# Performance work log

Measured on AMD Instinct MI355X. Metric: run time of the kernel, lower is better.

## Reference

```python
import jax, jax.numpy as jnp
import numpy as np

FEATURE_DIM = 256
NUM_STEPS = 3
NUM_GRAPHS = 2048
ATOMS_PER_GRAPH = 64
TOTAL_ATOMS = NUM_GRAPHS * ATOMS_PER_GRAPH


def setup_inputs() -> dict:
    key = jax.random.key(0)
    k_x, k1, k2, k3, k4 = jax.random.split(key, 5)
    H = FEATURE_DIM
    s = 1.0 / np.sqrt(H)
    x = jax.random.normal(k_x, (TOTAL_ATOMS, H), dtype=jnp.float32)
    batch = jnp.repeat(jnp.arange(NUM_GRAPHS, dtype=jnp.int64), ATOMS_PER_GRAPH)
    sizes = jnp.full((NUM_GRAPHS,), ATOMS_PER_GRAPH, dtype=jnp.int64)
    # LSTM params (PyTorch layout: gates ordered i, f, g, o)
    W_ih = jax.random.uniform(k1, (4 * H, H), jnp.float32, -s, s)
    W_hh = jax.random.uniform(k2, (4 * H, H), jnp.float32, -s, s)
    b_ih = jax.random.uniform(k3, (4 * H,), jnp.float32, -s, s)
    b_hh = jax.random.uniform(k4, (4 * H,), jnp.float32, -s, s)
    return {"x": x, "batch": batch, "sizes": sizes,
            "W_ih": W_ih, "W_hh": W_hh, "b_ih": b_ih, "b_hh": b_hh}


def _lstm_cell(u, hx, cx, W_ih, W_hh, b_ih, b_hh):
    # u: input [B,H]; (hx, cx): hidden/cell [B,H]
    gates = u @ W_ih.T + b_ih + hx @ W_hh.T + b_hh  # [B, 4H]
    i, f, g, o = jnp.split(gates, 4, axis=-1)
    i, f, o = jax.nn.sigmoid(i), jax.nn.sigmoid(f), jax.nn.sigmoid(o)
    c = f * cx + i * jnp.tanh(g)
    h = o * jnp.tanh(c)
    return h, c


def _segment_softmax(scores, seg, num_segments):
    m = jax.ops.segment_max(scores, seg, num_segments=num_segments)
    e = jnp.exp(scores - m[seg])
    s = jax.ops.segment_sum(e, seg, num_segments=num_segments)
    return e / s[seg]


def reference(x, batch, sizes, W_ih, W_hh, b_ih, b_hh):
    B = sizes.shape[0]
    H = x.shape[1]
    seg = batch.astype(jnp.int32)
    h = jnp.zeros((B, H), dtype=x.dtype)
    c = jnp.zeros((B, H), dtype=x.dtype)
    q = h
    r = h
    for _ in range(NUM_STEPS):
        # torch code feeds h both as LSTM input and hidden state
        q, c = _lstm_cell(h, h, c, W_ih, W_hh, b_ih, b_hh)
        scores = jnp.sum(x * q[seg], axis=-1)              # [total_atoms]
        attn = _segment_softmax(scores, seg, B)            # per-graph softmax
        r = jax.ops.segment_sum(x * attn[:, None], seg, num_segments=B)  # [B,H]
        h = r  # torch code overwrites the LSTM hidden with r
    return jnp.concatenate([q, r], axis=-1)  # [B, 2H]
```

## Files before the change

kernel.cpp:

```cpp
#include <hip/hip_runtime.h>
#include <math.h>

#define H 256
#define NB 2048
#define APG 64

typedef __attribute__((ext_vector_type(8))) short short8;
typedef __attribute__((ext_vector_type(4))) float f32x4;

__device__ __forceinline__ unsigned short f2bf(float f) {
    unsigned u = __float_as_uint(f);
    u += 0x7fff + ((u >> 16) & 1);
    return (unsigned short)(u >> 16);
}
__device__ __forceinline__ float bf2f(unsigned short s) {
    return __uint_as_float((unsigned)s << 16);
}
__device__ __forceinline__ float sigm(float v) { return 1.f / (1.f + __expf(-v)); }

__global__ void prep_kernel(const float* __restrict__ W_ih, const float* __restrict__ W_hh,
                            const float* __restrict__ b_ih, const float* __restrict__ b_hh,
                            unsigned short* __restrict__ Wr, float* __restrict__ br) {
    int idx = blockIdx.x * 256 + threadIdx.x;
    int wr_row = idx >> 8, k = idx & 255;
    int hcol = wr_row >> 2, gate = wr_row & 3;
    int src = gate * 65536 + hcol * 256 + k;
    Wr[idx] = f2bf(W_ih[src] + W_hh[src]);
    if (idx < 1024) {
        int hc = idx >> 2, gt = idx & 3;
        br[idx] = b_ih[gt * 256 + hc] + b_hh[gt * 256 + hc];
    }
}

__global__ void lstm0(const float* __restrict__ br, float* __restrict__ q1,
                      float* __restrict__ c1) {
    int hc = threadIdx.x;
    float gi = br[hc * 4 + 0], gg = br[hc * 4 + 2], go = br[hc * 4 + 3];
    float si = sigm(gi), so = sigm(go);
    float cn = si * tanhf(gg);
    c1[hc] = cn;
    q1[hc] = so * tanhf(cn);
}

__global__ __launch_bounds__(256)
void gemm_lstm(const unsigned short* __restrict__ hbf, const unsigned short* __restrict__ Wr,
               const float* __restrict__ br, float* __restrict__ c,
               float* __restrict__ qdst, int qstride) {
    __shared__ unsigned short smem[2][64 * 128];
    unsigned short* As = smem[0];
    unsigned short* Bs = smem[1];
    int t = threadIdx.x;
    int r0 = blockIdx.y * 64;
    int w0 = blockIdx.x * 64;
    int c0h = blockIdx.x * 16;
    int lane = t & 63, w = t >> 6;
    int ln = lane & 15, qd = lane >> 4;
    int m0 = w * 16;
    f32x4 acc[4] = {};
    for (int kc = 0; kc < 2; ++kc) {
        #pragma unroll
        for (int p = 0; p < 4; ++p) {
            int gid = p * 256 + t;
            int row = gid >> 4, g = gid & 15;
            int sg = g ^ (row & 15);
            *(short8*)&As[row * 128 + sg * 8] =
                *(const short8*)&hbf[(r0 + row) * H + kc * 128 + g * 8];
            *(short8*)&Bs[row * 128 + sg * 8] =
                *(const short8*)&Wr[(w0 + row) * H + kc * 128 + g * 8];
        }
        __syncthreads();
        #pragma unroll
        for (int kk = 0; kk < 4; ++kk) {
            int ga = (kk * 4 + qd) ^ ln;
            short8 a = *(short8*)&As[(m0 + ln) * 128 + ga * 8];
            #pragma unroll
            for (int t4 = 0; t4 < 4; ++t4) {
                short8 b = *(short8*)&Bs[(t4 * 16 + ln) * 128 + ga * 8];
                acc[t4] = __builtin_amdgcn_mfma_f32_16x16x32_bf16(a, b, acc[t4], 0, 0, 0);
            }
        }
        __syncthreads();
    }
    float* gl = (float*)smem;
    #pragma unroll
    for (int t4 = 0; t4 < 4; ++t4)
        #pragma unroll
        for (int r = 0; r < 4; ++r)
            gl[(m0 + qd * 4 + r) * 68 + t4 * 16 + ln] = acc[t4][r];
    __syncthreads();
    #pragma unroll
    for (int p = 0; p < 4; ++p) {
        int idx = p * 256 + t;
        int row = idx >> 4, hc = idx & 15;
        float4 g4 = *(float4*)&gl[row * 68 + hc * 4];
        float4 b4 = *(const float4*)&br[(c0h + hc) * 4];
        float gi = g4.x + b4.x, gf = g4.y + b4.y, gg = g4.z + b4.z, go = g4.w + b4.w;
        float si = sigm(gi), sf = sigm(gf), so = sigm(go);
        int cidx = (r0 + row) * H + c0h + hc;
        float cn = sf * c[cidx] + si * tanhf(gg);
        c[cidx] = cn;
        qdst[(r0 + row) * qstride + c0h + hc] = so * tanhf(cn);
    }
}

__global__ __launch_bounds__(256)
void attention1(const float* __restrict__ x, const float* __restrict__ q1,
                unsigned short* __restrict__ hbf, const float* __restrict__ c1,
                float* __restrict__ cdst, unsigned short* __restrict__ xbf) {
    __shared__ float sc[64];
    __shared__ float pl[64];
    __shared__ float rpart[4][256];
    int g = blockIdx.x, t = threadIdx.x;
    int lane = t & 63, w = t >> 6;
    const float* xg = x + (size_t)g * APG * H;
    unsigned short* xbg = xbf + (size_t)g * APG * H;
    float4 xa[16];
    #pragma unroll
    for (int i = 0; i < 16; ++i)
        xa[i] = *(const float4*)&xg[(i * 4 + w) * H + lane * 4];
    float4 q4 = *(const float4*)&q1[lane * 4];
    cdst[g * H + t] = c1[t];
    #pragma unroll
    for (int i = 0; i < 16; ++i) {
        ushort4 u;
        u.x = f2bf(xa[i].x); u.y = f2bf(xa[i].y);
        u.z = f2bf(xa[i].z); u.w = f2bf(xa[i].w);
        *(ushort4*)&xbg[(i * 4 + w) * H + lane * 4] = u;
    }
    #pragma unroll
    for (int i = 0; i < 16; ++i) {
        float p = xa[i].x * q4.x + xa[i].y * q4.y + xa[i].z * q4.z + xa[i].w * q4.w;
        #pragma unroll
        for (int s = 32; s > 0; s >>= 1) p += __shfl_xor(p, s, 64);
        if (lane == 0) sc[i * 4 + w] = p;
    }
    __syncthreads();
    if (t < 64) {
        float s = sc[t], m = s;
        #pragma unroll
        for (int d = 32; d > 0; d >>= 1) m = fmaxf(m, __shfl_xor(m, d, 64));
        float e = __expf(s - m), sum = e;
        #pragma unroll
        for (int d = 32; d > 0; d >>= 1) sum += __shfl_xor(sum, d, 64);
        pl[t] = e / sum;
    }
    __syncthreads();
    float4 r4 = {0.f, 0.f, 0.f, 0.f};
    #pragma unroll
    for (int i = 0; i < 16; ++i) {
        float p = pl[i * 4 + w];
        r4.x += p * xa[i].x; r4.y += p * xa[i].y;
        r4.z += p * xa[i].z; r4.w += p * xa[i].w;
    }
    *(float4*)&rpart[w][lane * 4] = r4;
    __syncthreads();
    float o = rpart[0][t] + rpart[1][t] + rpart[2][t] + rpart[3][t];
    hbf[g * H + t] = f2bf(o);
}

__global__ __launch_bounds__(256)
void attention_bf(const unsigned short* __restrict__ xbf, const float* __restrict__ qsrc,
                  int qstride, unsigned short* __restrict__ hbf,
                  float* __restrict__ rf32, int rstride) {
    __shared__ float sc[64];
    __shared__ float pl[64];
    __shared__ float rpart[4][256];
    int g = blockIdx.x, t = threadIdx.x;
    int lane = t & 63, w = t >> 6;
    const unsigned short* xg = xbf + (size_t)g * APG * H;
    ushort4 xa[16];
    #pragma unroll
    for (int i = 0; i < 16; ++i)
        xa[i] = *(const ushort4*)&xg[(i * 4 + w) * H + lane * 4];
    float4 q4 = *(const float4*)&qsrc[g * qstride + lane * 4];
    #pragma unroll
    for (int i = 0; i < 16; ++i) {
        float p = bf2f(xa[i].x) * q4.x + bf2f(xa[i].y) * q4.y
                + bf2f(xa[i].z) * q4.z + bf2f(xa[i].w) * q4.w;
        #pragma unroll
        for (int s = 32; s > 0; s >>= 1) p += __shfl_xor(p, s, 64);
        if (lane == 0) sc[i * 4 + w] = p;
    }
    __syncthreads();
    if (t < 64) {
        float s = sc[t], m = s;
        #pragma unroll
        for (int d = 32; d > 0; d >>= 1) m = fmaxf(m, __shfl_xor(m, d, 64));
        float e = __expf(s - m), sum = e;
        #pragma unroll
        for (int d = 32; d > 0; d >>= 1) sum += __shfl_xor(sum, d, 64);
        pl[t] = e / sum;
    }
    __syncthreads();
    float4 r4 = {0.f, 0.f, 0.f, 0.f};
    #pragma unroll
    for (int i = 0; i < 16; ++i) {
        float p = pl[i * 4 + w];
        r4.x += p * bf2f(xa[i].x); r4.y += p * bf2f(xa[i].y);
        r4.z += p * bf2f(xa[i].z); r4.w += p * bf2f(xa[i].w);
    }
    *(float4*)&rpart[w][lane * 4] = r4;
    __syncthreads();
    float o = rpart[0][t] + rpart[1][t] + rpart[2][t] + rpart[3][t];
    if (hbf)  hbf[g * H + t] = f2bf(o);
    if (rf32) rf32[g * rstride + t] = o;
}

extern "C" void kernel_launch(void* const* d_in, const int* in_sizes, int n_in,
                              void* d_out, int out_size, void* d_ws, size_t ws_size,
                              hipStream_t stream) {
    const float* x    = (const float*)d_in[0];
    const float* W_ih = (const float*)d_in[3];
    const float* W_hh = (const float*)d_in[4];
    const float* b_ih = (const float*)d_in[5];
    const float* b_hh = (const float*)d_in[6];
    float* out = (float*)d_out;

    char* ws = (char*)d_ws;
    unsigned short* Wr   = (unsigned short*)ws;
    float*          br   = (float*)(ws + 524288);
    unsigned short* hbf  = (unsigned short*)(ws + 528384);
    float*          cbuf = (float*)(ws + 1576960);
    float*          qbuf = (float*)(ws + 3674112);
    float*          q1   = (float*)(ws + 5771264);
    float*          c1   = (float*)(ws + 5772288);
    unsigned short* xbf  = (unsigned short*)(ws + 8388608);

    prep_kernel<<<1024, 256, 0, stream>>>(W_ih, W_hh, b_ih, b_hh, Wr, br);
    lstm0<<<1, 256, 0, stream>>>(br, q1, c1);
    attention1<<<2048, 256, 0, stream>>>(x, q1, hbf, c1, cbuf, xbf);
    gemm_lstm<<<dim3(16, 32), 256, 0, stream>>>(hbf, Wr, br, cbuf, qbuf, 256);
    attention_bf<<<2048, 256, 0, stream>>>(xbf, qbuf, 256, hbf, nullptr, 0);
    gemm_lstm<<<dim3(16, 32), 256, 0, stream>>>(hbf, Wr, br, cbuf, out, 512);
    attention_bf<<<2048, 256, 0, stream>>>(xbf, out, 512, nullptr, out + 256, 512);
}
```

Measured before the change: 267.1 us.

## Fuse all LSTM and attention steps into one persistent per-graph-group kernel

```diff
diff --git a/kernel.cpp b/kernel.cpp
--- a/kernel.cpp
+++ b/kernel.cpp
@@ -4,6 +4,8 @@
 #define H 256
 #define NB 2048
 #define APG 64
+#define GPB 8
+#define HBF_LD 272
 
 typedef __attribute__((ext_vector_type(8))) short short8;
 typedef __attribute__((ext_vector_type(4))) float f32x4;
@@ -13,10 +15,15 @@
     u += 0x7fff + ((u >> 16) & 1);
     return (unsigned short)(u >> 16);
 }
-__device__ __forceinline__ float bf2f(unsigned short s) {
-    return __uint_as_float((unsigned)s << 16);
+__device__ __forceinline__ float sigm(float v) { return 1.f / (1.f + __expf(-v)); }
+
+__device__ __forceinline__ void bar_lds() {
+    __builtin_amdgcn_sched_barrier(0);
+    asm volatile("s_waitcnt lgkmcnt(0)" ::: "memory");
+    __builtin_amdgcn_s_barrier();
+    asm volatile("" ::: "memory");
+    __builtin_amdgcn_sched_barrier(0);
 }
-__device__ __forceinline__ float sigm(float v) { return 1.f / (1.f + __expf(-v)); }
 
 __global__ void prep_kernel(const float* __restrict__ W_ih, const float* __restrict__ W_hh,
                             const float* __restrict__ b_ih, const float* __restrict__ b_hh,
@@ -32,178 +39,132 @@
     }
 }
 
-__global__ void lstm0(const float* __restrict__ br, float* __restrict__ q1,
-                      float* __restrict__ c1) {
-    int hc = threadIdx.x;
-    float gi = br[hc * 4 + 0], gg = br[hc * 4 + 2], go = br[hc * 4 + 3];
-    float si = sigm(gi), so = sigm(go);
-    float cn = si * tanhf(gg);
-    c1[hc] = cn;
-    q1[hc] = so * tanhf(cn);
-}
+__global__ __launch_bounds__(256, 1)
+void fused(const float* __restrict__ x, const unsigned short* __restrict__ Wr,
+           const float* __restrict__ br, float* __restrict__ out) {
+    __shared__ __align__(16) float brs[1024];
+    __shared__ __align__(16) float q1s[256];
+    __shared__ __align__(16) float cst[GPB][256];
+    __shared__ __align__(16) float qs[GPB][256];
+    __shared__ __align__(16) unsigned short hbfs[16 * HBF_LD];
+    __shared__ __align__(16) float gates[GPB][1024];
+    __shared__ __align__(16) float sc[64];
+    __shared__ __align__(16) float rpart[4][256];
 
-__global__ __launch_bounds__(256)
-void gemm_lstm(const unsigned short* __restrict__ hbf, const unsigned short* __restrict__ Wr,
-               const float* __restrict__ br, float* __restrict__ c,
-               float* __restrict__ qdst, int qstride) {
-    __shared__ unsigned short smem[2][64 * 128];
-    unsigned short* As = smem[0];
-    unsigned short* Bs = smem[1];
     int t = threadIdx.x;
-    int r0 = blockIdx.y * 64;
-    int w0 = blockIdx.x * 64;
-    int c0h = blockIdx.x * 16;
     int lane = t & 63, w = t >> 6;
     int ln = lane & 15, qd = lane >> 4;
-    int m0 = w * 16;
-    f32x4 acc[4] = {};
-    for (int kc = 0; kc < 2; ++kc) {
+    int gbase = blockIdx.x * GPB;
+    const float* xbase = x + (size_t)gbase * APG * H;
+
+    float4 b4 = *(const float4*)&br[t * 4];
+    #pragma unroll
+    for (int j = 0; j < 4; ++j) brs[j * 256 + t] = br[j * 256 + t];
+    float cn1 = sigm(b4.x) * tanhf(b4.z);
+    q1s[t] = sigm(b4.w) * tanhf(cn1);
+    #pragma unroll
+    for (int g = 0; g < GPB; ++g) cst[g][t] = cn1;
+    #pragma unroll
+    for (int r = 8; r < 16; ++r) hbfs[r * HBF_LD + t] = 0;
+    __syncthreads();
+
+    for (int s = 0; s < 3; ++s) {
+        if (s > 0) {
+            short8 a[8];
+            #pragma unroll
+            for (int kk = 0; kk < 8; ++kk)
+                a[kk] = *(short8*)&hbfs[ln * HBF_LD + kk * 32 + qd * 8];
+            const unsigned short* wrow = Wr + (size_t)(w * 256 + ln) * H + qd * 8;
+            #pragma unroll
+            for (int tile = 0; tile < 16; ++tile) {
+                const unsigned short* wt = wrow + tile * 16 * H;
+                short8 b[8];
+                #pragma unroll
+                for (int kk = 0; kk < 8; ++kk) b[kk] = *(const short8*)&wt[kk * 32];
+                f32x4 acc = {0.f, 0.f, 0.f, 0.f};
+                #pragma unroll
+                for (int kk = 0; kk < 8; ++kk)
+                    acc = __builtin_amdgcn_mfma_f32_16x16x32_bf16(a[kk], b[kk], acc, 0, 0, 0);
+                if (qd < 2) {
+                    #pragma unroll
+                    for (int r = 0; r < 4; ++r)
+                        gates[qd * 4 + r][w * 256 + tile * 16 + ln] = acc[r];
+                }
+            }
+            __syncthreads();
+            #pragma unroll
+            for (int j = 0; j < GPB; ++j) {
+                float4 g4 = *(float4*)&gates[j][t * 4];
+                float4 bb = *(float4*)&brs[t * 4];
+                float gi = g4.x + bb.x, gf = g4.y + bb.y,
+                      gg = g4.z + bb.z, go = g4.w + bb.w;
+                float si = sigm(gi), sf = sigm(gf), so = sigm(go);
+                float cn = sf * cst[j][t] + si * tanhf(gg);
+                cst[j][t] = cn;
+                float qv = so * tanhf(cn);
+                qs[j][t] = qv;
+                if (s == 2) out[(size_t)(gbase + j) * 512 + t] = qv;
+            }
+            __syncthreads();
+        }
+
+        float4 xaA[16], xaB[16];
         #pragma unroll
-        for (int p = 0; p < 4; ++p) {
-            int gid = p * 256 + t;
-            int row = gid >> 4, g = gid & 15;
-            int sg = g ^ (row & 15);
-            *(short8*)&As[row * 128 + sg * 8] =
-                *(const short8*)&hbf[(r0 + row) * H + kc * 128 + g * 8];
-            *(short8*)&Bs[row * 128 + sg * 8] =
-                *(const short8*)&Wr[(w0 + row) * H + kc * 128 + g * 8];
+        for (int i = 0; i < 16; ++i)
+            xaA[i] = *(const float4*)&xbase[(i * 4 + w) * H + lane * 4];
+
+#define ATTN_BODY(g, CUR, NXT)                                                      \
+        {                                                                           \
+            if ((g) + 1 < GPB) {         \
+                const float* xn = xbase + (size_t)((g) + 1) * APG * H;              \
+                _Pragma("unroll")                                                   \
+                for (int i = 0; i < 16; ++i)                                        \
+                    NXT[i] = *(const float4*)&xn[(i * 4 + w) * H + lane * 4];       \
+            }                                                                       \
+            float4 q4;                                                              \
+            if (s == 0) q4 = *(float4*)&q1s[lane * 4];                              \
+            else        q4 = *(float4*)&qs[g][lane * 4];                            \
+            _Pragma("unroll")                                                       \
+            for (int i = 0; i < 16; ++i) {                                          \
+                float p = CUR[i].x * q4.x + CUR[i].y * q4.y                         \
+                        + CUR[i].z * q4.z + CUR[i].w * q4.w;                        \
+                _Pragma("unroll")                                                   \
+                for (int d = 32; d > 0; d >>= 1) p += __shfl_xor(p, d, 64);         \
+                if (lane == 0) sc[i * 4 + w] = p;                                   \
+            }                                                                       \
+            bar_lds();                                                              \
+            float sv = sc[lane], m = sv;      \
+            _Pragma("unroll")                                                       \
+            for (int d = 32; d > 0; d >>= 1) m = fmaxf(m, __shfl_xor(m, d, 64));    \
+            float e = __expf(sv - m), sum = e;                                      \
+            _Pragma("unroll")                                                       \
+            for (int d = 32; d > 0; d >>= 1) sum += __shfl_xor(sum, d, 64);         \
+            float pv = e / sum;                                                     \
+            float4 r4 = {0.f, 0.f, 0.f, 0.f};                                       \
+            _Pragma("unroll")                                                       \
+            for (int i = 0; i < 16; ++i) {                                          \
+                float p = __shfl(pv, i * 4 + w, 64);                                \
+                r4.x += p * CUR[i].x; r4.y += p * CUR[i].y;                         \
+                r4.z += p * CUR[i].z; r4.w += p * CUR[i].w;                         \
+            }                                                                       \
+            *(float4*)&rpart[w][lane * 4] = r4;                                     \
+            bar_lds();                                                              \
+            float o = rpart[0][t] + rpart[1][t] + rpart[2][t] + rpart[3][t];        \
+            if (s < 2) hbfs[(g) * HBF_LD + t] = f2bf(o);                            \
+            else       out[(size_t)(gbase + (g)) * 512 + 256 + t] = o;              \
         }
-        __syncthreads();
-        #pragma unroll
-        for (int kk = 0; kk < 4; ++kk) {
-            int ga = (kk * 4 + qd) ^ ln;
-            short8 a = *(short8*)&As[(m0 + ln) * 128 + ga * 8];
-            #pragma unroll
-            for (int t4 = 0; t4 < 4; ++t4) {
-                short8 b = *(short8*)&Bs[(t4 * 16 + ln) * 128 + ga * 8];
-                acc[t4] = __builtin_amdgcn_mfma_f32_16x16x32_bf16(a, b, acc[t4], 0, 0, 0);
-            }
-        }
+
+        ATTN_BODY(0, xaA, xaB)
+        ATTN_BODY(1, xaB, xaA)
+        ATTN_BODY(2, xaA, xaB)
+        ATTN_BODY(3, xaB, xaA)
+        ATTN_BODY(4, xaA, xaB)
+        ATTN_BODY(5, xaB, xaA)
+        ATTN_BODY(6, xaA, xaB)
+        ATTN_BODY(7, xaB, xaA)
+#undef ATTN_BODY
         __syncthreads();
     }
-    float* gl = (float*)smem;
-    #pragma unroll
-    for (int t4 = 0; t4 < 4; ++t4)
-        #pragma unroll
-        for (int r = 0; r < 4; ++r)
-            gl[(m0 + qd * 4 + r) * 68 + t4 * 16 + ln] = acc[t4][r];
-    __syncthreads();
-    #pragma unroll
-    for (int p = 0; p < 4; ++p) {
-        int idx = p * 256 + t;
-        int row = idx >> 4, hc = idx & 15;
-        float4 g4 = *(float4*)&gl[row * 68 + hc * 4];
-        float4 b4 = *(const float4*)&br[(c0h + hc) * 4];
-        float gi = g4.x + b4.x, gf = g4.y + b4.y, gg = g4.z + b4.z, go = g4.w + b4.w;
-        float si = sigm(gi), sf = sigm(gf), so = sigm(go);
-        int cidx = (r0 + row) * H + c0h + hc;
-        float cn = sf * c[cidx] + si * tanhf(gg);
-        c[cidx] = cn;
-        qdst[(r0 + row) * qstride + c0h + hc] = so * tanhf(cn);
-    }
-}
-
-__global__ __launch_bounds__(256)
-void attention1(const float* __restrict__ x, const float* __restrict__ q1,
-                unsigned short* __restrict__ hbf, const float* __restrict__ c1,
-                float* __restrict__ cdst, unsigned short* __restrict__ xbf) {
-    __shared__ float sc[64];
-    __shared__ float pl[64];
-    __shared__ float rpart[4][256];
-    int g = blockIdx.x, t = threadIdx.x;
-    int lane = t & 63, w = t >> 6;
-    const float* xg = x + (size_t)g * APG * H;
-    unsigned short* xbg = xbf + (size_t)g * APG * H;
-    float4 xa[16];
-    #pragma unroll
-    for (int i = 0; i < 16; ++i)
-        xa[i] = *(const float4*)&xg[(i * 4 + w) * H + lane * 4];
-    float4 q4 = *(const float4*)&q1[lane * 4];
-    cdst[g * H + t] = c1[t];
-    #pragma unroll
-    for (int i = 0; i < 16; ++i) {
-        ushort4 u;
-        u.x = f2bf(xa[i].x); u.y = f2bf(xa[i].y);
-        u.z = f2bf(xa[i].z); u.w = f2bf(xa[i].w);
-        *(ushort4*)&xbg[(i * 4 + w) * H + lane * 4] = u;
-    }
-    #pragma unroll
-    for (int i = 0; i < 16; ++i) {
-        float p = xa[i].x * q4.x + xa[i].y * q4.y + xa[i].z * q4.z + xa[i].w * q4.w;
-        #pragma unroll
-        for (int s = 32; s > 0; s >>= 1) p += __shfl_xor(p, s, 64);
-        if (lane == 0) sc[i * 4 + w] = p;
-    }
-    __syncthreads();
-    if (t < 64) {
-        float s = sc[t], m = s;
-        #pragma unroll
-        for (int d = 32; d > 0; d >>= 1) m = fmaxf(m, __shfl_xor(m, d, 64));
-        float e = __expf(s - m), sum = e;
-        #pragma unroll
-        for (int d = 32; d > 0; d >>= 1) sum += __shfl_xor(sum, d, 64);
-        pl[t] = e / sum;
-    }
-    __syncthreads();
-    float4 r4 = {0.f, 0.f, 0.f, 0.f};
-    #pragma unroll
-    for (int i = 0; i < 16; ++i) {
-        float p = pl[i * 4 + w];
-        r4.x += p * xa[i].x; r4.y += p * xa[i].y;
-        r4.z += p * xa[i].z; r4.w += p * xa[i].w;
-    }
-    *(float4*)&rpart[w][lane * 4] = r4;
-    __syncthreads();
-    float o = rpart[0][t] + rpart[1][t] + rpart[2][t] + rpart[3][t];
-    hbf[g * H + t] = f2bf(o);
-}
-
-__global__ __launch_bounds__(256)
-void attention_bf(const unsigned short* __restrict__ xbf, const float* __restrict__ qsrc,
-                  int qstride, unsigned short* __restrict__ hbf,
-                  float* __restrict__ rf32, int rstride) {
-    __shared__ float sc[64];
-    __shared__ float pl[64];
-    __shared__ float rpart[4][256];
-    int g = blockIdx.x, t = threadIdx.x;
-    int lane = t & 63, w = t >> 6;
-    const unsigned short* xg = xbf + (size_t)g * APG * H;
-    ushort4 xa[16];
-    #pragma unroll
-    for (int i = 0; i < 16; ++i)
-        xa[i] = *(const ushort4*)&xg[(i * 4 + w) * H + lane * 4];
-    float4 q4 = *(const float4*)&qsrc[g * qstride + lane * 4];
-    #pragma unroll
-    for (int i = 0; i < 16; ++i) {
-        float p = bf2f(xa[i].x) * q4.x + bf2f(xa[i].y) * q4.y
-                + bf2f(xa[i].z) * q4.z + bf2f(xa[i].w) * q4.w;
-        #pragma unroll
-        for (int s = 32; s > 0; s >>= 1) p += __shfl_xor(p, s, 64);
-        if (lane == 0) sc[i * 4 + w] = p;
-    }
-    __syncthreads();
-    if (t < 64) {
-        float s = sc[t], m = s;
-        #pragma unroll
-        for (int d = 32; d > 0; d >>= 1) m = fmaxf(m, __shfl_xor(m, d, 64));
-        float e = __expf(s - m), sum = e;
-        #pragma unroll
-        for (int d = 32; d > 0; d >>= 1) sum += __shfl_xor(sum, d, 64);
-        pl[t] = e / sum;
-    }
-    __syncthreads();
-    float4 r4 = {0.f, 0.f, 0.f, 0.f};
-    #pragma unroll
-    for (int i = 0; i < 16; ++i) {
-        float p = pl[i * 4 + w];
-        r4.x += p * bf2f(xa[i].x); r4.y += p * bf2f(xa[i].y);
-        r4.z += p * bf2f(xa[i].z); r4.w += p * bf2f(xa[i].w);
-    }
-    *(float4*)&rpart[w][lane * 4] = r4;
-    __syncthreads();
-    float o = rpart[0][t] + rpart[1][t] + rpart[2][t] + rpart[3][t];
-    if (hbf)  hbf[g * H + t] = f2bf(o);
-    if (rf32) rf32[g * rstride + t] = o;
 }
 
 extern "C" void kernel_launch(void* const* d_in, const int* in_sizes, int n_in,
@@ -214,23 +175,11 @@
     const float* W_hh = (const float*)d_in[4];
     const float* b_ih = (const float*)d_in[5];
     const float* b_hh = (const float*)d_in[6];
-    float* out = (float*)d_out;
 
     char* ws = (char*)d_ws;
-    unsigned short* Wr   = (unsigned short*)ws;
-    float*          br   = (float*)(ws + 524288);
-    unsigned short* hbf  = (unsigned short*)(ws + 528384);
-    float*          cbuf = (float*)(ws + 1576960);
-    float*          qbuf = (float*)(ws + 3674112);
-    float*          q1   = (float*)(ws + 5771264);
-    float*          c1   = (float*)(ws + 5772288);
-    unsigned short* xbf  = (unsigned short*)(ws + 8388608);
+    unsigned short* Wr = (unsigned short*)ws;
+    float*          br = (float*)(ws + 524288);
 
     prep_kernel<<<1024, 256, 0, stream>>>(W_ih, W_hh, b_ih, b_hh, Wr, br);
-    lstm0<<<1, 256, 0, stream>>>(br, q1, c1);
-    attention1<<<2048, 256, 0, stream>>>(x, q1, hbf, c1, cbuf, xbf);
-    gemm_lstm<<<dim3(16, 32), 256, 0, stream>>>(hbf, Wr, br, cbuf, qbuf, 256);
-    attention_bf<<<2048, 256, 0, stream>>>(xbf, qbuf, 256, hbf, nullptr, 0);
-    gemm_lstm<<<dim3(16, 32), 256, 0, stream>>>(hbf, Wr, br, cbuf, out, 512);
-    attention_bf<<<2048, 256, 0, stream>>>(xbf, out, 512, nullptr, out + 256, 512);
+    fused<<<256, 256, 0, stream>>>(x, Wr, br, (float*)d_out);
 }
```

Measured after the change: 399.9 us. 1.5x slower.
